# Kernel tuning notes

Hardware: AMD Instinct MI355X
Metric: run time of the kernel (lower is better)

## Reference

```python
import jax, jax.numpy as jnp
import numpy as np

VOCAB, EMBED, HIDDEN, LAYERS = 32000, 512, 1024, 2
BATCH, SEQ = 32, 128


def gru_layer(x_tbe, h0, W_ih, W_hh, b_ih, b_hh):
    """x_tbe: [T,B,E_in]; h0: [B,H]. PyTorch GRU gate math."""
    # Precompute input-side gates for all timesteps (one big GEMM).
    gi = jnp.einsum('tbe,ge->tbg', x_tbe, W_ih) + b_ih  # [T,B,3H]

    def step(h, gi_t):
        gh = h @ W_hh.T + b_hh                      # [B,3H]
        i_r, i_z, i_n = jnp.split(gi_t, 3, axis=-1)
        h_r, h_z, h_n = jnp.split(gh, 3, axis=-1)
        r = jax.nn.sigmoid(i_r + h_r)
        z = jax.nn.sigmoid(i_z + h_z)
        n = jnp.tanh(i_n + r * h_n)
        h_new = (1.0 - z) * n + z * h
        return h_new, h_new

    hT, ys = jax.lax.scan(step, h0, gi)
    return ys, hT  # ys: [T,B,H]


def setup_inputs() -> dict:
    key = jax.random.key(0)
    ks = jax.random.split(key, 16)
    s = 0.02
    inp = {
        'inputs': jax.random.randint(ks[0], (BATCH, SEQ), 0, VOCAB),
        'lengths': jax.random.randint(ks[1], (BATCH,), 1, SEQ),
        'hidden': jax.random.normal(ks[2], (LAYERS, BATCH, HIDDEN), jnp.float32),
        'embed_table': jax.random.normal(ks[3], (VOCAB, EMBED), jnp.float32) * s,
        'W_ih_l0': jax.random.normal(ks[4], (3 * HIDDEN, EMBED), jnp.float32) * s,
        'W_hh_l0': jax.random.normal(ks[5], (3 * HIDDEN, HIDDEN), jnp.float32) * s,
        'b_ih_l0': jnp.zeros((3 * HIDDEN,), jnp.float32),
        'b_hh_l0': jnp.zeros((3 * HIDDEN,), jnp.float32),
        'W_ih_l1': jax.random.normal(ks[6], (3 * HIDDEN, HIDDEN), jnp.float32) * s,
        'W_hh_l1': jax.random.normal(ks[7], (3 * HIDDEN, HIDDEN), jnp.float32) * s,
        'b_ih_l1': jnp.zeros((3 * HIDDEN,), jnp.float32),
        'b_hh_l1': jnp.zeros((3 * HIDDEN,), jnp.float32),
        'W_out': jax.random.normal(ks[8], (VOCAB, HIDDEN), jnp.float32) * s,
        'b_out': jnp.zeros((VOCAB,), jnp.float32),
    }
    return inp


def reference(inputs, lengths, hidden, embed_table,
              W_ih_l0, W_hh_l0, b_ih_l0, b_hh_l0,
              W_ih_l1, W_hh_l1, b_ih_l1, b_hh_l1,
              W_out, b_out):
    # embedding: [B,S,E] -> time-major [S,B,E]
    x = embed_table[inputs].transpose(1, 0, 2)
    x, _ = gru_layer(x, hidden[0], W_ih_l0, W_hh_l0, b_ih_l0, b_hh_l0)
    x, _ = gru_layer(x, hidden[1], W_ih_l1, W_hh_l1, b_ih_l1, b_hh_l1)
    outputs = x.transpose(1, 0, 2)                   # [B,S,H]
    logits = outputs @ W_out.T + b_out               # [B,S,V]
    return logits
```

## Files before the change

kernel.cpp:

```cpp
#include <hip/hip_runtime.h>
#include <hip/hip_bf16.h>
#include <stdint.h>

#define T_SEQ 128
#define NBATCH 32
#define EMBED 512
#define HID 1024
#define NVOCAB 32000
#define NBLK 256

typedef float f32x4 __attribute__((ext_vector_type(4)));
typedef _Float16 f16x8 __attribute__((ext_vector_type(8)));

__device__ __forceinline__ unsigned short f2h(float f) {
  _Float16 h = (_Float16)f;
  return __builtin_bit_cast(unsigned short, h);
}
__device__ __forceinline__ float sigm(float x) {
  return 1.0f / (1.0f + __expf(-x));
}
__device__ __forceinline__ float tanh_fast(float x) {
  return 2.0f / (1.0f + __expf(-2.0f * x)) - 1.0f;
}
__device__ __forceinline__ unsigned umin4(unsigned a, unsigned b, unsigned c, unsigned d) {
  unsigned x = a < b ? a : b;
  unsigned y = c < d ? c : d;
  return x < y ? x : y;
}

__global__ void k_zero(unsigned int* __restrict__ p, int n) {
  int i = blockIdx.x * blockDim.x + threadIdx.x;
  if (i < n) p[i] = 0;
}

__global__ void k_f32_to_f16(const float4* __restrict__ in,
                             ushort4* __restrict__ out, int n4) {
  int i = blockIdx.x * blockDim.x + threadIdx.x;
  int stride = gridDim.x * blockDim.x;
  for (; i < n4; i += stride) {
    float4 v = in[i];
    ushort4 o;
    o.x = f2h(v.x); o.y = f2h(v.y); o.z = f2h(v.z); o.w = f2h(v.w);
    out[i] = o;
  }
}

__global__ void k_embed(const int* __restrict__ tok, const float* __restrict__ table,
                        ushort4* __restrict__ A0) {
  int tid = blockIdx.x * 256 + threadIdx.x;
  int m = tid >> 7, kq = tid & 127;
  int b = m & 31, t = m >> 5;
  int tk = tok[b * T_SEQ + t];
  float4 v = *(const float4*)(table + (size_t)tk * EMBED + kq * 4);
  ushort4 o;
  o.x = f2h(v.x); o.y = f2h(v.y); o.z = f2h(v.z); o.w = f2h(v.w);
  A0[tid] = o;
}

#define BM 128
#define BN 128
#define BKK 64

__global__ __launch_bounds__(256) void k_gemm_bt(
    const short* __restrict__ A,
    const short* __restrict__ B,
    float* __restrict__ C,
    const float* __restrict__ bias,
    int M, int N, int K, int permute)
{
  __shared__ __align__(16) short As[BM * BKK];
  __shared__ __align__(16) short Bs[BN * BKK];
  const int tid = threadIdx.x;
  const int w = tid >> 6, l = tid & 63;
  const int wr = w >> 1, wc = w & 1;
  const int bm = blockIdx.x * BM, bn = blockIdx.y * BN;
  const int l15 = l & 15, lkg = l >> 4;

  f32x4 acc[4][4] = {};

  for (int kt = 0; kt < K; kt += BKK) {
#pragma unroll
    for (int p = 0; p < 4; ++p) {
      int idx = p * 2048 + tid * 8;
      int r = idx >> 6, c = idx & 63;
      *(f16x8*)&As[idx] = *(const f16x8*)&A[(size_t)(bm + r) * K + kt + c];
      *(f16x8*)&Bs[idx] = *(const f16x8*)&B[(size_t)(bn + r) * K + kt + c];
    }
    __syncthreads();

#pragma unroll
    for (int ks = 0; ks < 2; ++ks) {
      f16x8 af[4], bfr[4];
#pragma unroll
      for (int mi = 0; mi < 4; ++mi)
        af[mi] = *(const f16x8*)&As[(wr * 64 + mi * 16 + l15) * BKK + ks * 32 + lkg * 8];
#pragma unroll
      for (int ni = 0; ni < 4; ++ni)
        bfr[ni] = *(const f16x8*)&Bs[(wc * 64 + ni * 16 + l15) * BKK + ks * 32 + lkg * 8];
#pragma unroll
      for (int mi = 0; mi < 4; ++mi)
#pragma unroll
        for (int ni = 0; ni < 4; ++ni)
          acc[mi][ni] = __builtin_amdgcn_mfma_f32_16x16x32_f16(
              af[mi], bfr[ni], acc[mi][ni], 0, 0, 0);
    }
    __syncthreads();
  }

  const int lr = lkg * 4;
#pragma unroll
  for (int mi = 0; mi < 4; ++mi) {
#pragma unroll
    for (int ni = 0; ni < 4; ++ni) {
      int col = bn + wc * 64 + ni * 16 + l15;
      float bv = bias ? bias[col] : 0.0f;
#pragma unroll
      for (int j = 0; j < 4; ++j) {
        int row = bm + wr * 64 + mi * 16 + lr + j;
        int orow = permute ? ((row & 31) * T_SEQ + (row >> 5)) : row;
        C[(size_t)orow * N + col] = acc[mi][ni][j] + bv;
      }
    }
  }
}

#define LK 1024
#define GNT 16

__global__ __launch_bounds__(512, 2) void k_gemm256(
    const short* __restrict__ A,
    const short* __restrict__ B,
    float* __restrict__ C,
    const float* __restrict__ bias,
    int N)
{
  __shared__ __align__(16) short As[2][256 * 64];
  __shared__ __align__(16) short Bs[2][256 * 64];

  const int tid = threadIdx.x;
  const int l = tid & 63, wid = tid >> 6;
  const int wm = wid >> 2, wn = wid & 3;
  const int l15 = l & 15, lkg = l >> 4;
  const int bm = blockIdx.x * 256, bn = blockIdx.y * 256;

  f32x4 acc[8][4] = {};

  auto stage_half = [&](int kt, int op, int half) {
    const short* G = op ? B : A;
    const int base_row = (op ? bn : bm) + half * 128;
    char* L = (char*)(op ? Bs[kt & 1] : As[kt & 1]) + half * 128 * 64 * 2;
#pragma unroll
    for (int p = 0; p < 2; ++p) {
      int chunk = p * 512 + tid;
      int Lbyte = chunk * 16;
      int r = Lbyte >> 7;
      int cb = Lbyte & 127;
      int scb = cb ^ ((r & 7) << 4);
      const char* src = (const char*)&G[(size_t)(base_row + r) * LK + kt * 64] + scb;
      char* dst = L + (p * 512 + wid * 64) * 16;
      __builtin_amdgcn_global_load_lds(
          (const __attribute__((address_space(1))) void*)src,
          (__attribute__((address_space(3))) void*)dst, 16, 0, 0);
    }
  };

  stage_half(0, 0, 0); stage_half(0, 0, 1);
  stage_half(0, 1, 0); stage_half(0, 1, 1);
  stage_half(1, 0, 0); stage_half(1, 0, 1);
  asm volatile("s_waitcnt vmcnt(4)" ::: "memory");
  __builtin_amdgcn_sched_barrier(0);
  __builtin_amdgcn_s_barrier();
  __builtin_amdgcn_sched_barrier(0);

  for (int kt = 0; kt < GNT; ++kt) {
    const char* bufA = (const char*)As[kt & 1];
    const char* bufB = (const char*)Bs[kt & 1];
    f16x8 afr[8][2];
    f16x8 bfr[2][2];

#define RD_A(mi_, ks_) \
    (*(const f16x8*)(bufA + ((wm * 128 + (mi_) * 16 + l15) * 128 + \
        (((ks_) * 64 + lkg * 16) ^ (((wm * 128 + (mi_) * 16 + l15) & 7) << 4)))))
#define RD_B(ni_, ks_) \
    (*(const f16x8*)(bufB + ((wn * 64 + (ni_) * 16 + l15) * 128 + \
        (((ks_) * 64 + lkg * 16) ^ (((wn * 64 + (ni_) * 16 + l15) & 7) << 4)))))

#define MFMA_QUAD(MI0, NI0) \
    __builtin_amdgcn_s_setprio(1); \
    _Pragma("unroll") \
    for (int ks = 0; ks < 2; ++ks) \
      _Pragma("unroll") \
      for (int i = 0; i < 4; ++i) \
        _Pragma("unroll") \
        for (int j = 0; j < 2; ++j) \
          acc[(MI0) + i][(NI0) + j] = __builtin_amdgcn_mfma_f32_16x16x32_f16( \
              afr[(MI0) + i][ks], bfr[j][ks], acc[(MI0) + i][(NI0) + j], 0, 0, 0); \
    __builtin_amdgcn_s_setprio(0);

#define PHASE_BARS() \
    __builtin_amdgcn_s_barrier(); __builtin_amdgcn_sched_barrier(0);

#pragma unroll
    for (int i = 0; i < 4; ++i) { afr[i][0] = RD_A(i, 0); afr[i][1] = RD_A(i, 1); }
#pragma unroll
    for (int j = 0; j < 2; ++j) { bfr[j][0] = RD_B(j, 0); bfr[j][1] = RD_B(j, 1); }
    if (kt + 1 < GNT) stage_half(kt + 1, 1, 0);
    PHASE_BARS();
    MFMA_QUAD(0, 0);
    PHASE_BARS();

#pragma unroll
    for (int i = 0; i < 4; ++i) { afr[4 + i][0] = RD_A(4 + i, 0); afr[4 + i][1] = RD_A(4 + i, 1); }
    if (kt + 1 < GNT) stage_half(kt + 1, 1, 1);
    PHASE_BARS();
    MFMA_QUAD(4, 0);
    PHASE_BARS();

#pragma unroll
    for (int j = 0; j < 2; ++j) { bfr[j][0] = RD_B(2 + j, 0); bfr[j][1] = RD_B(2 + j, 1); }
    if (kt + 2 < GNT) stage_half(kt + 2, 0, 0);
    PHASE_BARS();
    MFMA_QUAD(0, 2);
    PHASE_BARS();

    if (kt + 2 < GNT) stage_half(kt + 2, 0, 1);
    PHASE_BARS();
    MFMA_QUAD(4, 2);
    PHASE_BARS();

    if (kt + 1 < GNT) {
      if (kt + 2 < GNT) {
        asm volatile("s_waitcnt vmcnt(4)" ::: "memory");
      } else {
        asm volatile("s_waitcnt vmcnt(0)" ::: "memory");
      }
      __builtin_amdgcn_sched_barrier(0);
      __builtin_amdgcn_s_barrier();
      __builtin_amdgcn_sched_barrier(0);
    }
#undef RD_A
#undef RD_B
#undef MFMA_QUAD
#undef PHASE_BARS
  }

  const int lr = lkg * 4;
#pragma unroll
  for (int mi = 0; mi < 8; ++mi) {
#pragma unroll
    for (int ni = 0; ni < 4; ++ni) {
      int col = bn + wn * 64 + ni * 16 + l15;
      float bv = bias[col];
#pragma unroll
      for (int j = 0; j < 4; ++j) {
        int row = bm + wm * 128 + mi * 16 + lr + j;
        int orow = (row & 31) * T_SEQ + (row >> 5);
        C[(size_t)orow * N + col] = acc[mi][ni][j] + bv;
      }
    }
  }
}

__global__ __launch_bounds__(384, 2) void k_gru_fused(
    const float* __restrict__ gi0,
    const float* __restrict__ Whh0,
    const float* __restrict__ bhh0,
    const float* __restrict__ Wih1,
    const float* __restrict__ bih1,
    const float* __restrict__ Whh1,
    const float* __restrict__ bhh1,
    const _Float16* __restrict__ h0i,
    const _Float16* __restrict__ h1i,
    _Float16* __restrict__ ys0f,
    _Float16* __restrict__ ys1f,
    unsigned int* flg0,
    unsigned int* flg1)
{
  __shared__ float bufIH[2][3][2][64];

  const int tid = threadIdx.x;
  const int l = tid & 63;
  const int w = tid >> 6;
  const int role = w >> 1, nt = w & 1;
  const int bid = blockIdx.x;
  const int j0 = bid * 4;

  const int row16 = l & 15;
  const int jjr = row16 >> 2, gate = row16 & 3;
  const int koct = l >> 4;

  const int b_out = nt * 16 + (l & 15);
  const int j_out = j0 + (l >> 4);
  const int jj_even = (((l >> 4) & 1) == 0);

  const float* Wsrc = (role == 0) ? Whh0 : ((role == 1) ? Wih1 : Whh1);
  f16x8 af[32];
  if (gate < 3) {
    const float* wrow = Wsrc + (size_t)(gate * HID + j0 + jjr) * HID;
#pragma unroll
    for (int c = 0; c < 32; ++c) {
      float4 p0 = *(const float4*)(wrow + c * 32 + koct * 8);
      float4 p1 = *(const float4*)(wrow + c * 32 + koct * 8 + 4);
      f16x8 v = { (_Float16)p0.x, (_Float16)p0.y, (_Float16)p0.z, (_Float16)p0.w,
                  (_Float16)p1.x, (_Float16)p1.y, (_Float16)p1.z, (_Float16)p1.w };
      af[c] = v;
    }
  } else {
#pragma unroll
    for (int c = 0; c < 32; ++c) {
      f16x8 z = { (_Float16)0.f, (_Float16)0.f, (_Float16)0.f, (_Float16)0.f,
                  (_Float16)0.f, (_Float16)0.f, (_Float16)0.f, (_Float16)0.f };
      af[c] = z;
    }
  }

  float bR = 0.f, bZ = 0.f, bN = 0.f, biR = 0.f, biZ = 0.f, biN = 0.f;
  if (role == 0) {
    bR = bhh0[j_out]; bZ = bhh0[HID + j_out]; bN = bhh0[2 * HID + j_out];
  } else if (role == 2) {
    bR = bhh1[j_out]; bZ = bhh1[HID + j_out]; bN = bhh1[2 * HID + j_out];
    biR = bih1[j_out]; biZ = bih1[HID + j_out]; biN = bih1[2 * HID + j_out];
  }

  const int bfragOff = b_out * 2048 + koct * 16;

  for (int s = 0; s <= T_SEQ + 1; ++s) {
    float pre_ir = 0.f, pre_iz = 0.f, pre_in = 0.f;
    if (role == 0 && s < T_SEQ) {
      const float* gib = gi0 + (size_t)(s * NBATCH + b_out) * 3072 + j_out;
      pre_ir = gib[0]; pre_iz = gib[HID]; pre_in = gib[2 * HID];
    }

    if (w == 0) {
      unsigned need0 = (s >= 1 && s <= T_SEQ) ? (unsigned)s : 0u;
      unsigned need1 = (s >= 3) ? (unsigned)(s - 2) : 0u;
      if ((need0 | need1) != 0u) {
        const unsigned* f0 = flg0 + l * 4;
        const unsigned* f1 = flg1 + l * 4;
        for (;;) {
          unsigned m0 = 0xffffffffu, m1 = 0xffffffffu;
          if (need0) {
            unsigned a0 = __hip_atomic_load(f0 + 0, __ATOMIC_RELAXED, __HIP_MEMORY_SCOPE_AGENT);
            unsigned a1 = __hip_atomic_load(f0 + 1, __ATOMIC_RELAXED, __HIP_MEMORY_SCOPE_AGENT);
            unsigned a2 = __hip_atomic_load(f0 + 2, __ATOMIC_RELAXED, __HIP_MEMORY_SCOPE_AGENT);
            unsigned a3 = __hip_atomic_load(f0 + 3, __ATOMIC_RELAXED, __HIP_MEMORY_SCOPE_AGENT);
            m0 = umin4(a0, a1, a2, a3);
          }
          if (need1) {
            unsigned a0 = __hip_atomic_load(f1 + 0, __ATOMIC_RELAXED, __HIP_MEMORY_SCOPE_AGENT);
            unsigned a1 = __hip_atomic_load(f1 + 1, __ATOMIC_RELAXED, __HIP_MEMORY_SCOPE_AGENT);
            unsigned a2 = __hip_atomic_load(f1 + 2, __ATOMIC_RELAXED, __HIP_MEMORY_SCOPE_AGENT);
            unsigned a3 = __hip_atomic_load(f1 + 3, __ATOMIC_RELAXED, __HIP_MEMORY_SCOPE_AGENT);
            m1 = umin4(a0, a1, a2, a3);
          }
          if (__all(m0 >= need0 && m1 >= need1)) break;
          __builtin_amdgcn_s_sleep(1);
        }
        asm volatile("" ::: "memory");
      }
    }
    __syncthreads();

    if (role == 0 && s < T_SEQ) {
      const _Float16* hsrc = (s == 0) ? h0i : (ys0f + (size_t)(s - 1) * NBATCH * HID);
      const char* hb = (const char*)hsrc + bfragOff;
      f32x4 acc0 = {}, acc1 = {};
#pragma unroll
      for (int c = 0; c < 32; c += 2) {
        f16x8 bf0 = *(const f16x8*)(hb + c * 64);
        f16x8 bf1 = *(const f16x8*)(hb + c * 64 + 64);
        acc0 = __builtin_amdgcn_mfma_f32_16x16x32_f16(af[c], bf0, acc0, 0, 0, 0);
        acc1 = __builtin_amdgcn_mfma_f32_16x16x32_f16(af[c + 1], bf1, acc1, 0, 0, 0);
      }
      f32x4 acc = acc0 + acc1;

      float hp = (float)((s == 0) ? h0i[b_out * HID + j_out]
                                  : ys0f[(size_t)((s - 1) * NBATCH + b_out) * HID + j_out]);
      float r = sigm(pre_ir + acc[0] + bR);
      float z = sigm(pre_iz + acc[1] + bZ);
      float n = tanh_fast(pre_in + r * (acc[2] + bN));
      float hnew = (1.0f - z) * n + z * hp;

      unsigned bits = (unsigned)f2h(hnew);
      unsigned hi = __shfl_down(bits, 16);
      if (jj_even) {
        unsigned packed = (bits & 0xffffu) | (hi << 16);
        __hip_atomic_store((unsigned*)(ys0f + (size_t)(s * NBATCH + b_out) * HID + j_out),
                           packed, __ATOMIC_RELAXED, __HIP_MEMORY_SCOPE_AGENT);
      }
    }

    if (role == 1 && s >= 1 && s <= T_SEQ) {
      const _Float16* hsrc = ys0f + (size_t)(s - 1) * NBATCH * HID;
      const char* hb = (const char*)hsrc + bfragOff;
      f32x4 acc0 = {}, acc1 = {};
#pragma unroll
      for (int c = 0; c < 32; c += 2) {
        f16x8 bf0 = *(const f16x8*)(hb + c * 64);
        f16x8 bf1 = *(const f16x8*)(hb + c * 64 + 64);
        acc0 = __builtin_amdgcn_mfma_f32_16x16x32_f16(af[c], bf0, acc0, 0, 0, 0);
        acc1 = __builtin_amdgcn_mfma_f32_16x16x32_f16(af[c + 1], bf1, acc1, 0, 0, 0);
      }
      f32x4 acc = acc0 + acc1;
      bufIH[s & 1][0][nt][l] = acc[0];
      bufIH[s & 1][1][nt][l] = acc[1];
      bufIH[s & 1][2][nt][l] = acc[2];
    }

    if (role == 2 && s >= 2) {
      const int t1 = s - 2;
      const _Float16* hsrc = (t1 == 0) ? h1i : (ys1f + (size_t)(t1 - 1) * NBATCH * HID);
      const char* hb = (const char*)hsrc + bfragOff;
      f32x4 acc0 = {}, acc1 = {};
#pragma unroll
      for (int c = 0; c < 32; c += 2) {
        f16x8 bf0 = *(const f16x8*)(hb + c * 64);
        f16x8 bf1 = *(const f16x8*)(hb + c * 64 + 64);
        acc0 = __builtin_amdgcn_mfma_f32_16x16x32_f16(af[c], bf0, acc0, 0, 0, 0);
        acc1 = __builtin_amdgcn_mfma_f32_16x16x32_f16(af[c + 1], bf1, acc1, 0, 0, 0);
      }
      f32x4 acc = acc0 + acc1;

      const int par = (s - 1) & 1;
      float ihR = bufIH[par][0][nt][l] + biR;
      float ihZ = bufIH[par][1][nt][l] + biZ;
      float ihN = bufIH[par][2][nt][l] + biN;
      float hp = (float)((t1 == 0) ? h1i[b_out * HID + j_out]
                                   : ys1f[(size_t)((t1 - 1) * NBATCH + b_out) * HID + j_out]);
      float r = sigm(ihR + acc[0] + bR);
      float z = sigm(ihZ + acc[1] + bZ);
      float n = tanh_fast(ihN + r * (acc[2] + bN));
      float hnew = (1.0f - z) * n + z * hp;

      unsigned bits = (unsigned)f2h(hnew);
      unsigned hi = __shfl_down(bits, 16);
      if (jj_even) {
        unsigned packed = (bits & 0xffffu) | (hi << 16);
        __hip_atomic_store((unsigned*)(ys1f + (size_t)(t1 * NBATCH + b_out) * HID + j_out),
                           packed, __ATOMIC_RELAXED, __HIP_MEMORY_SCOPE_AGENT);
      }
    }

    __syncthreads();

    if (tid == 0) {
      if (s < T_SEQ)
        __hip_atomic_store(&flg0[bid], (unsigned)(s + 1), __ATOMIC_RELAXED, __HIP_MEMORY_SCOPE_AGENT);
      if (s >= 2)
        __hip_atomic_store(&flg1[bid], (unsigned)(s - 1), __ATOMIC_RELAXED, __HIP_MEMORY_SCOPE_AGENT);
    }
  }
}

extern "C" void kernel_launch(void* const* d_in, const int* in_sizes, int n_in,
                              void* d_out, int out_size, void* d_ws, size_t ws_size,
                              hipStream_t stream)
{
  const int*   inputs = (const int*)d_in[0];
  const float* hidden = (const float*)d_in[2];
  const float* table  = (const float*)d_in[3];
  const float* Wih0   = (const float*)d_in[4];
  const float* Whh0   = (const float*)d_in[5];
  const float* bih0   = (const float*)d_in[6];
  const float* bhh0   = (const float*)d_in[7];
  const float* Wih1   = (const float*)d_in[8];
  const float* Whh1   = (const float*)d_in[9];
  const float* bih1   = (const float*)d_in[10];
  const float* bhh1   = (const float*)d_in[11];
  const float* Wout   = (const float*)d_in[12];
  const float* bout   = (const float*)d_in[13];
  float* out = (float*)d_out;

  char* ws = (char*)d_ws;
  size_t off = 0;
  auto alloc = [&](size_t bytes) {
    void* p = ws + off;
    off += (bytes + 255) & ~(size_t)255;
    return p;
  };
  float*     gi0  = (float*)alloc((size_t)4096 * 3072 * 4);
  _Float16*  ys0f = (_Float16*)alloc((size_t)4096 * 1024 * 2);
  _Float16*  ys1f = (_Float16*)alloc((size_t)4096 * 1024 * 2);
  short*     A0   = (short*)alloc((size_t)4096 * 512 * 2);
  short*     B0   = (short*)alloc((size_t)3072 * 512 * 2);
  short*     B2   = (short*)alloc((size_t)32000 * 1024 * 2);
  _Float16*  hcat = (_Float16*)alloc((size_t)2 * 32 * 1024 * 2);
  _Float16*  h0i  = hcat;
  _Float16*  h1i  = hcat + 32 * 1024;
  unsigned int* flg0 = (unsigned int*)alloc(256 * 4);
  unsigned int* flg1 = (unsigned int*)alloc(256 * 4);

  k_zero<<<1, 512, 0, stream>>>(flg0, 512);

  k_f32_to_f16<<<1024, 256, 0, stream>>>((const float4*)Wih0, (ushort4*)B0, 3072 * 512 / 4);
  k_f32_to_f16<<<2048, 256, 0, stream>>>((const float4*)Wout, (ushort4*)B2, 32000 * 1024 / 4);
  k_f32_to_f16<<<64, 256, 0, stream>>>((const float4*)hidden, (ushort4*)hcat, 2 * 32 * 1024 / 4);
  k_embed<<<2048, 256, 0, stream>>>(inputs, table, (ushort4*)A0);

  dim3 g0(32, 24);
  k_gemm_bt<<<g0, 256, 0, stream>>>(A0, B0, gi0, bih0, 4096, 3072, 512, 0);

  {
    void* kargs[] = {
      (void*)&gi0, (void*)&Whh0, (void*)&bhh0,
      (void*)&Wih1, (void*)&bih1, (void*)&Whh1, (void*)&bhh1,
      (void*)&h0i, (void*)&h1i, (void*)&ys0f, (void*)&ys1f,
      (void*)&flg0, (void*)&flg1
    };
    hipError_t e = hipLaunchCooperativeKernel((const void*)k_gru_fused, dim3(NBLK),
                                              dim3(384), kargs, 0, stream);
    if (e != hipSuccess) {
      (void)hipGetLastError();
      k_gru_fused<<<dim3(NBLK), dim3(384), 0, stream>>>(
          gi0, Whh0, bhh0, Wih1, bih1, Whh1, bhh1,
          h0i, h1i, ys0f, ys1f, flg0, flg1);
    }
  }

  dim3 g2(16, 125);
  k_gemm256<<<g2, 512, 0, stream>>>((const short*)ys1f, B2, out, bout, NVOCAB);
}
```

Baseline: 1.470 ms.

## Fuse layer-0 input GEMM and Wout conversion into persistent GRU kernel

Removes the separate layer-0 input-projection GEMM and its large fp32 gi0 buffer. Each role-0 warp now computes its input gates on the fly with MFMA from register-resident fp16 Wih0 fragments, running a few timesteps ahead into an LDS ring buffer. It also folds the Wout fp32-to-fp16 conversion into the idle warps of the recurrent kernel, one row per step. This trades two launches and a large memory round-trip for extra registers (af0[16]) and extra work per step inside the latency-critical recurrence.

Measured after the change: 1.754 ms. 19.3% more time.

```diff
diff --git a/kernel.cpp b/kernel.cpp
--- a/kernel.cpp
+++ b/kernel.cpp
@@ -8,6 +8,7 @@
 #define HID 1024
 #define NVOCAB 32000
 #define NBLK 256
+#define LA 6
 
 typedef float f32x4 __attribute__((ext_vector_type(4)));
 typedef _Float16 f16x8 __attribute__((ext_vector_type(8)));
@@ -55,73 +56,6 @@
   ushort4 o;
   o.x = f2h(v.x); o.y = f2h(v.y); o.z = f2h(v.z); o.w = f2h(v.w);
   A0[tid] = o;
-}
-
-#define BM 128
-#define BN 128
-#define BKK 64
-
-__global__ __launch_bounds__(256) void k_gemm_bt(
-    const short* __restrict__ A,
-    const short* __restrict__ B,
-    float* __restrict__ C,
-    const float* __restrict__ bias,
-    int M, int N, int K, int permute)
-{
-  __shared__ __align__(16) short As[BM * BKK];
-  __shared__ __align__(16) short Bs[BN * BKK];
-  const int tid = threadIdx.x;
-  const int w = tid >> 6, l = tid & 63;
-  const int wr = w >> 1, wc = w & 1;
-  const int bm = blockIdx.x * BM, bn = blockIdx.y * BN;
-  const int l15 = l & 15, lkg = l >> 4;
-
-  f32x4 acc[4][4] = {};
-
-  for (int kt = 0; kt < K; kt += BKK) {
-#pragma unroll
-    for (int p = 0; p < 4; ++p) {
-      int idx = p * 2048 + tid * 8;
-      int r = idx >> 6, c = idx & 63;
-      *(f16x8*)&As[idx] = *(const f16x8*)&A[(size_t)(bm + r) * K + kt + c];
-      *(f16x8*)&Bs[idx] = *(const f16x8*)&B[(size_t)(bn + r) * K + kt + c];
-    }
-    __syncthreads();
-
-#pragma unroll
-    for (int ks = 0; ks < 2; ++ks) {
-      f16x8 af[4], bfr[4];
-#pragma unroll
-      for (int mi = 0; mi < 4; ++mi)
-        af[mi] = *(const f16x8*)&As[(wr * 64 + mi * 16 + l15) * BKK + ks * 32 + lkg * 8];
-#pragma unroll
-      for (int ni = 0; ni < 4; ++ni)
-        bfr[ni] = *(const f16x8*)&Bs[(wc * 64 + ni * 16 + l15) * BKK + ks * 32 + lkg * 8];
-#pragma unroll
-      for (int mi = 0; mi < 4; ++mi)
-#pragma unroll
-        for (int ni = 0; ni < 4; ++ni)
-          acc[mi][ni] = __builtin_amdgcn_mfma_f32_16x16x32_f16(
-              af[mi], bfr[ni], acc[mi][ni], 0, 0, 0);
-    }
-    __syncthreads();
-  }
-
-  const int lr = lkg * 4;
-#pragma unroll
-  for (int mi = 0; mi < 4; ++mi) {
-#pragma unroll
-    for (int ni = 0; ni < 4; ++ni) {
-      int col = bn + wc * 64 + ni * 16 + l15;
-      float bv = bias ? bias[col] : 0.0f;
-#pragma unroll
-      for (int j = 0; j < 4; ++j) {
-        int row = bm + wr * 64 + mi * 16 + lr + j;
-        int orow = permute ? ((row & 31) * T_SEQ + (row >> 5)) : row;
-        C[(size_t)orow * N + col] = acc[mi][ni][j] + bv;
-      }
-    }
-  }
 }
 
 #define LK 1024
@@ -262,7 +196,9 @@
 }
 
 __global__ __launch_bounds__(384, 2) void k_gru_fused(
-    const float* __restrict__ gi0,
+    const short* __restrict__ A0,
+    const float* __restrict__ Wih0,
+    const float* __restrict__ bih0,
     const float* __restrict__ Whh0,
     const float* __restrict__ bhh0,
     const float* __restrict__ Wih1,
@@ -273,10 +209,13 @@
     const _Float16* __restrict__ h1i,
     _Float16* __restrict__ ys0f,
     _Float16* __restrict__ ys1f,
+    const float* __restrict__ Wout,
+    unsigned short* __restrict__ B2,
     unsigned int* flg0,
     unsigned int* flg1)
 {
   __shared__ float bufIH[2][3][2][64];
+  __shared__ __align__(16) f32x4 ring[2][8][64];
 
   const int tid = threadIdx.x;
   const int l = tid & 63;
@@ -314,21 +253,66 @@
     }
   }
 
+  f16x8 af0[16];
+  if (role == 0 && gate < 3) {
+    const float* wrow = Wih0 + (size_t)(gate * HID + j0 + jjr) * EMBED;
+#pragma unroll
+    for (int c = 0; c < 16; ++c) {
+      float4 p0 = *(const float4*)(wrow + c * 32 + koct * 8);
+      float4 p1 = *(const float4*)(wrow + c * 32 + koct * 8 + 4);
+      f16x8 v = { (_Float16)p0.x, (_Float16)p0.y, (_Float16)p0.z, (_Float16)p0.w,
+                  (_Float16)p1.x, (_Float16)p1.y, (_Float16)p1.z, (_Float16)p1.w };
+      af0[c] = v;
+    }
+  } else {
+#pragma unroll
+    for (int c = 0; c < 16; ++c) {
+      f16x8 z = { (_Float16)0.f, (_Float16)0.f, (_Float16)0.f, (_Float16)0.f,
+                  (_Float16)0.f, (_Float16)0.f, (_Float16)0.f, (_Float16)0.f };
+      af0[c] = z;
+    }
+  }
+
   float bR = 0.f, bZ = 0.f, bN = 0.f, biR = 0.f, biZ = 0.f, biN = 0.f;
+  float g0R = 0.f, g0Z = 0.f, g0N = 0.f;
   if (role == 0) {
     bR = bhh0[j_out]; bZ = bhh0[HID + j_out]; bN = bhh0[2 * HID + j_out];
+    g0R = bih0[j_out]; g0Z = bih0[HID + j_out]; g0N = bih0[2 * HID + j_out];
   } else if (role == 2) {
     bR = bhh1[j_out]; bZ = bhh1[HID + j_out]; bN = bhh1[2 * HID + j_out];
     biR = bih1[j_out]; biZ = bih1[HID + j_out]; biN = bih1[2 * HID + j_out];
   }
 
   const int bfragOff = b_out * 2048 + koct * 16;
+  const int a0fragOff = b_out * 1024 + koct * 16;
+
+  auto gi0_tile = [&](int tp) {
+    const char* ab = (const char*)A0 + (size_t)tp * 32 * 1024 + a0fragOff;
+    f32x4 g0 = {}, g1 = {};
+#pragma unroll
+    for (int c = 0; c < 16; c += 2) {
+      f16x8 b0 = *(const f16x8*)(ab + c * 64);
+      f16x8 b1 = *(const f16x8*)(ab + c * 64 + 64);
+      g0 = __builtin_amdgcn_mfma_f32_16x16x32_f16(af0[c], b0, g0, 0, 0, 0);
+      g1 = __builtin_amdgcn_mfma_f32_16x16x32_f16(af0[c + 1], b1, g1, 0, 0, 0);
+    }
+    ring[nt][tp & 7][l] = g0 + g1;
+  };
+
+  if (role == 0) {
+#pragma unroll
+    for (int tp = 0; tp < LA; ++tp) gi0_tile(tp);
+  }
 
   for (int s = 0; s <= T_SEQ + 1; ++s) {
-    float pre_ir = 0.f, pre_iz = 0.f, pre_in = 0.f;
-    if (role == 0 && s < T_SEQ) {
-      const float* gib = gi0 + (size_t)(s * NBATCH + b_out) * 3072 + j_out;
-      pre_ir = gib[0]; pre_iz = gib[HID]; pre_in = gib[2 * HID];
+    if (role == 0 && s + LA < T_SEQ) gi0_tile(s + LA);
+    if (w >= 2 && s < 125) {
+      int row = bid * 125 + s;
+      int t4 = (w - 2) * 64 + l;
+      float4 v = *(const float4*)(Wout + (size_t)row * 1024 + t4 * 4);
+      ushort4 o;
+      o.x = f2h(v.x); o.y = f2h(v.y); o.z = f2h(v.z); o.w = f2h(v.w);
+      *(ushort4*)(B2 + (size_t)row * 1024 + t4 * 4) = o;
     }
 
     if (w == 0) {
@@ -373,12 +357,13 @@
         acc1 = __builtin_amdgcn_mfma_f32_16x16x32_f16(af[c + 1], bf1, acc1, 0, 0, 0);
       }
       f32x4 acc = acc0 + acc1;
+      f32x4 gi = ring[nt][s & 7][l];
 
       float hp = (float)((s == 0) ? h0i[b_out * HID + j_out]
                                   : ys0f[(size_t)((s - 1) * NBATCH + b_out) * HID + j_out]);
-      float r = sigm(pre_ir + acc[0] + bR);
-      float z = sigm(pre_iz + acc[1] + bZ);
-      float n = tanh_fast(pre_in + r * (acc[2] + bN));
+      float r = sigm(gi[0] + g0R + acc[0] + bR);
+      float z = sigm(gi[1] + g0Z + acc[1] + bZ);
+      float n = tanh_fast(gi[2] + g0N + r * (acc[2] + bN));
       float hnew = (1.0f - z) * n + z * hp;
 
       unsigned bits = (unsigned)f2h(hnew);
@@ -478,12 +463,10 @@
     off += (bytes + 255) & ~(size_t)255;
     return p;
   };
-  float*     gi0  = (float*)alloc((size_t)4096 * 3072 * 4);
   _Float16*  ys0f = (_Float16*)alloc((size_t)4096 * 1024 * 2);
   _Float16*  ys1f = (_Float16*)alloc((size_t)4096 * 1024 * 2);
   short*     A0   = (short*)alloc((size_t)4096 * 512 * 2);
-  short*     B0   = (short*)alloc((size_t)3072 * 512 * 2);
-  short*     B2   = (short*)alloc((size_t)32000 * 1024 * 2);
+  unsigned short* B2 = (unsigned short*)alloc((size_t)32000 * 1024 * 2);
   _Float16*  hcat = (_Float16*)alloc((size_t)2 * 32 * 1024 * 2);
   _Float16*  h0i  = hcat;
   _Float16*  h1i  = hcat + 32 * 1024;
@@ -492,19 +475,16 @@
 
   k_zero<<<1, 512, 0, stream>>>(flg0, 512);
 
-  k_f32_to_f16<<<1024, 256, 0, stream>>>((const float4*)Wih0, (ushort4*)B0, 3072 * 512 / 4);
-  k_f32_to_f16<<<2048, 256, 0, stream>>>((const float4*)Wout, (ushort4*)B2, 32000 * 1024 / 4);
   k_f32_to_f16<<<64, 256, 0, stream>>>((const float4*)hidden, (ushort4*)hcat, 2 * 32 * 1024 / 4);
   k_embed<<<2048, 256, 0, stream>>>(inputs, table, (ushort4*)A0);
 
-  dim3 g0(32, 24);
-  k_gemm_bt<<<g0, 256, 0, stream>>>(A0, B0, gi0, bih0, 4096, 3072, 512, 0);
-
   {
     void* kargs[] = {
-      (void*)&gi0, (void*)&Whh0, (void*)&bhh0,
+      (void*)&A0, (void*)&Wih0, (void*)&bih0,
+      (void*)&Whh0, (void*)&bhh0,
       (void*)&Wih1, (void*)&bih1, (void*)&Whh1, (void*)&bhh1,
       (void*)&h0i, (void*)&h1i, (void*)&ys0f, (void*)&ys1f,
+      (void*)&Wout, (void*)&B2,
       (void*)&flg0, (void*)&flg1
     };
     hipError_t e = hipLaunchCooperativeKernel((const void*)k_gru_fused, dim3(NBLK),
@@ -512,11 +492,11 @@
     if (e != hipSuccess) {
       (void)hipGetLastError();
       k_gru_fused<<<dim3(NBLK), dim3(384), 0, stream>>>(
-          gi0, Whh0, bhh0, Wih1, bih1, Whh1, bhh1,
-          h0i, h1i, ys0f, ys1f, flg0, flg1);
+          (const short*)A0, Wih0, bih0, Whh0, bhh0, Wih1, bih1, Whh1, bhh1,
+          h0i, h1i, ys0f, ys1f, Wout, B2, flg0, flg1);
     }
   }
 
   dim3 g2(16, 125);
-  k_gemm256<<<g2, 512, 0, stream>>>((const short*)ys1f, B2, out, bout, NVOCAB);
-}
+  k_gemm256<<<g2, 512, 0, stream>>>((const short*)ys1f, (const short*)B2, out, bout, NVOCAB);
+}
```
